# Kernel tuning notes

Measured on AMD Instinct MI355X. Metric: run time of the kernel, lower is better.

Reference implementation:

```python
import jax, jax.numpy as jnp
import numpy as np

B, S, DIN, DQ, DK, NGL = 4, 8192, 512, 512, 512, 64


def setup_inputs() -> dict:
    key = jax.random.key(0)
    ks = jax.random.split(key, 10)
    q = jax.random.normal(ks[0], (B, S, DIN), dtype=jnp.float32)
    k = jax.random.normal(ks[1], (B, S, DIN), dtype=jnp.float32)
    v = jax.random.normal(ks[2], (B, S, DIN), dtype=jnp.float32)
    sc_in = 1.0 / np.sqrt(DIN)
    Wq = jax.random.normal(ks[3], (DQ, DIN), dtype=jnp.float32) * sc_in
    bq = jax.random.normal(ks[4], (DQ,), dtype=jnp.float32) * 0.01
    Wk = jax.random.normal(ks[5], (DK, DIN), dtype=jnp.float32) * sc_in
    bk = jax.random.normal(ks[6], (DK,), dtype=jnp.float32) * 0.01
    Wv = jax.random.normal(ks[7], (DK, DIN), dtype=jnp.float32) * sc_in
    bv = jax.random.normal(ks[8], (DK,), dtype=jnp.float32) * 0.01
    # deterministic stand-in for random.sample(range(DK), NGL): unique indices
    rng = np.random.default_rng(0)
    global_tokens = jnp.asarray(rng.choice(DK, size=NGL, replace=False), dtype=jnp.int32)
    return {"q": q, "k": k, "v": v, "Wq": Wq, "bq": bq, "Wk": Wk, "bk": bk,
            "Wv": Wv, "bv": bv, "global_tokens": global_tokens}


def _make_mask(global_tokens):
    # mask[a, b] = -inf iff a < b and neither a nor b is a global token
    idx = jnp.arange(DK)
    glb = jnp.zeros((DK,), dtype=bool).at[global_tokens].set(True)
    cond = (idx[:, None] < idx[None, :]) & (~glb[:, None]) & (~glb[None, :])
    return jnp.where(cond, -jnp.inf, 0.0).astype(jnp.float32)  # [DQ, DK]


def reference(q, k, v, Wq, bq, Wk, bk, Wv, bv, global_tokens):
    Q = q @ Wq.T + bq            # [B, S, DQ]
    K = k @ Wk.T + bk            # [B, S, DK]
    V = v @ Wv.T + bv            # [B, S, DK]
    # num = Q^T K contracting over the sequence axis -> [B, DQ, DK]
    num = jnp.einsum('bsq,bsk->bqk', Q, K)
    mask = _make_mask(global_tokens)
    denom = jnp.asarray(DK, jnp.float32) ** 0.5
    attn = jax.nn.softmax((num + mask) / denom, axis=-1)  # [B, DQ, DK]
    # attn @ V^T -> [B, DQ, S]
    out = jnp.einsum('bqk,bsk->bqs', attn, V)
    return out
```

## Files before the change

kernel.cpp:

```cpp
#include <hip/hip_runtime.h>
#include <stdint.h>

typedef short short8 __attribute__((ext_vector_type(8)));
typedef short short4v __attribute__((ext_vector_type(4)));
typedef float f32x4 __attribute__((ext_vector_type(4)));
typedef unsigned short ushort_t;

__device__ __forceinline__ void barrier_lds(){
  asm volatile("s_waitcnt lgkmcnt(0)\n\ts_barrier" ::: "memory");
}

__device__ __forceinline__ unsigned short bf16_rne(float x){
  unsigned int u = __float_as_uint(x);
  return (unsigned short)((u + 0x7FFFu + ((u >> 16) & 1u)) >> 16);
}
__device__ __forceinline__ unsigned cvt_pk(float a, float b){
  unsigned r;
  asm("v_cvt_pk_bf16_f32 %0, %1, %2" : "=v"(r) : "v"(a), "v"(b));
  return r;
}
__device__ __forceinline__ void split4(float a0, float a1, float a2, float a3,
                                       unsigned &h0, unsigned &h1,
                                       unsigned &l0, unsigned &l1){
  h0 = cvt_pk(a0, a1); h1 = cvt_pk(a2, a3);
  float f0 = __uint_as_float(h0 << 16), f1 = __uint_as_float(h0 & 0xFFFF0000u);
  float f2 = __uint_as_float(h1 << 16), f3 = __uint_as_float(h1 & 0xFFFF0000u);
  l0 = cvt_pk(a0 - f0, a1 - f1); l1 = cvt_pk(a2 - f2, a3 - f3);
}
__device__ __forceinline__ uint4 hi8(float4 x, float4 y){
  uint4 h; h.x = cvt_pk(x.x, x.y); h.y = cvt_pk(x.z, x.w);
  h.z = cvt_pk(y.x, y.y); h.w = cvt_pk(y.z, y.w); return h;
}
__device__ __forceinline__ void split8(float4 x, float4 y, uint4 &h, uint4 &l){
  split4(x.x, x.y, x.z, x.w, h.x, h.y, l.x, l.y);
  split4(y.x, y.y, y.z, y.w, h.z, h.w, l.z, l.w);
}
__device__ __forceinline__ short8 comb(short4v a, short4v b){
  short8 r; r[0]=a[0]; r[1]=a[1]; r[2]=a[2]; r[3]=a[3];
  r[4]=b[0]; r[5]=b[1]; r[6]=b[2]; r[7]=b[3]; return r;
}

template<int TS, int ABF, int BBF, int NT, int EPI, int OB>
__global__ __launch_bounds__(256, 2) void gemm_bt(
    const void* __restrict__ Av, const void* __restrict__ Bv,
    void* __restrict__ Cv, const float* __restrict__ cvec,
    int tn, int K, int lda, int ldb, int ldc,
    long sA, long sB, long sC, long scv)
{
  const int bz = blockIdx.y;
  const int mt = blockIdx.x / tn, nt = blockIdx.x % tn;
  const int m0 = mt * TS, n0 = nt * TS;

  constexpr int MI   = TS / 64;
  constexpr int ROWE = TS * 32;
  constexpr int PL   = (NT == 3) ? 2 * ROWE : ROWE;
  constexpr int TBYT = 4 * PL;
  constexpr int SB   = (2 * TBYT > 16384) ? 2 * TBYT : 16384;
  constexpr int EL   = (TS == 128) ? 16 : 8;
  __shared__ __align__(16) char SMEM[SB];
  short* Ah  = (short*)SMEM;
  short* Bh2 = (short*)(SMEM + TBYT);
  float* EP  = (float*)SMEM;

  const int t = threadIdx.x;
  const int lane = t & 63, wid = t >> 6;
  const int rowS = (TS == 128) ? (t >> 1) : (t >> 2);
  const int kh   = (TS == 128) ? (t & 1)  : (t & 3);
  const int wr = wid >> 1, wc = wid & 1;
  const int fr = lane & 15, fg = lane >> 4;

  f32x4 acc[2*MI][2*MI];
  const f32x4 Z = {0.f, 0.f, 0.f, 0.f};
  #pragma unroll
  for (int i = 0; i < 2*MI; i++)
    #pragma unroll
    for (int j = 0; j < 2*MI; j++) acc[i][j] = Z;

  const int wbase = rowS * 32;
  const int sw = (rowS >> 1) & 3;
  const int i0 = wbase + ((((TS == 128) ? (kh << 1) : kh) ^ sw) << 3);
  const int i1 = (TS == 128) ? (wbase + ((((kh << 1) + 1) ^ sw) << 3)) : 0;

  const float*    Afp = (const float*)Av    + sA * bz + (long)(m0 + rowS) * lda + kh * EL;
  const ushort_t* Abp = (const ushort_t*)Av + sA * bz + (long)(m0 + rowS) * lda + kh * EL;
  const float*    Bfp = (const float*)Bv    + sB * bz + (long)(n0 + rowS) * ldb + kh * EL;
  const ushort_t* Bbp = (const ushort_t*)Bv + sB * bz + (long)(n0 + rowS) * ldb + kh * EL;

  struct Pf { float4 v[4]; };
  struct Ps { short8 v[2]; };
  Pf Af[2], Bf[2]; Ps As8[2], Bs8[2];

  auto loadA = [&](int s, int kk){
    if (ABF == 0){
      const float4* p = (const float4*)(Afp + kk);
      Af[s].v[0] = p[0]; Af[s].v[1] = p[1];
      if (TS == 128){ Af[s].v[2] = p[2]; Af[s].v[3] = p[3]; }
    } else {
      const short8* p = (const short8*)(Abp + kk);
      As8[s].v[0] = p[0]; if (TS == 128) As8[s].v[1] = p[1];
    }
  };
  auto loadB = [&](int s, int kk){
    if (BBF == 0){
      const float4* p = (const float4*)(Bfp + kk);
      Bf[s].v[0] = p[0]; Bf[s].v[1] = p[1];
      if (TS == 128){ Bf[s].v[2] = p[2]; Bf[s].v[3] = p[3]; }
    } else {
      const short8* p = (const short8*)(Bbp + kk);
      Bs8[s].v[0] = p[0]; if (TS == 128) Bs8[s].v[1] = p[1];
    }
  };

  auto stage = [&](int s){
    const int off = s * PL;
    if (ABF == 0){
      if (NT == 3){
        uint4 h0, l0; split8(Af[s].v[0], Af[s].v[1], h0, l0);
        *(uint4*)&Ah[off + i0] = h0; *(uint4*)&Ah[off + i0 + ROWE] = l0;
        if (TS == 128){
          uint4 h1, l1; split8(Af[s].v[2], Af[s].v[3], h1, l1);
          *(uint4*)&Ah[off + i1] = h1; *(uint4*)&Ah[off + i1 + ROWE] = l1;
        }
      } else {
        *(uint4*)&Ah[off + i0] = hi8(Af[s].v[0], Af[s].v[1]);
        if (TS == 128) *(uint4*)&Ah[off + i1] = hi8(Af[s].v[2], Af[s].v[3]);
      }
    } else {
      *(short8*)&Ah[off + i0] = As8[s].v[0];
      if (TS == 128) *(short8*)&Ah[off + i1] = As8[s].v[1];
    }
    if (BBF == 0){
      if (NT == 3){
        uint4 h0, l0; split8(Bf[s].v[0], Bf[s].v[1], h0, l0);
        *(uint4*)&Bh2[off + i0] = h0; *(uint4*)&Bh2[off + i0 + ROWE] = l0;
        if (TS == 128){
          uint4 h1, l1; split8(Bf[s].v[2], Bf[s].v[3], h1, l1);
          *(uint4*)&Bh2[off + i1] = h1; *(uint4*)&Bh2[off + i1 + ROWE] = l1;
        }
      } else {
        *(uint4*)&Bh2[off + i0] = hi8(Bf[s].v[0], Bf[s].v[1]);
        if (TS == 128) *(uint4*)&Bh2[off + i1] = hi8(Bf[s].v[2], Bf[s].v[3]);
      }
    } else {
      *(short8*)&Bh2[off + i0] = Bs8[s].v[0];
      if (TS == 128) *(short8*)&Bh2[off + i1] = Bs8[s].v[1];
    }
  };

  loadA(0, 0); loadB(0, 0); loadA(1, 32); loadB(1, 32);

  for (int k0 = 0; k0 < K; k0 += 64){
    barrier_lds();
    stage(0);
    { int kn = (k0 + 64 < K) ? (k0 + 64) : k0;       loadA(0, kn); loadB(0, kn); }
    stage(1);
    { int kn = (k0 + 64 < K) ? (k0 + 96) : (k0 + 32); loadA(1, kn); loadB(1, kn); }
    barrier_lds();

    #pragma unroll
    for (int s = 0; s < 2; s++){
      const int off = s * PL;
      short8 fa[2*MI], fb[2*MI], fal[2*MI], fbl[2*MI];
      #pragma unroll
      for (int mi = 0; mi < 2*MI; mi++){
        int r = wr * (32*MI) + mi * 16 + fr;
        int idx = off + r * 32 + ((fg ^ ((r >> 1) & 3)) << 3);
        fa[mi] = *(const short8*)&Ah[idx];
        if (NT == 3) fal[mi] = *(const short8*)&Ah[idx + ROWE];
      }
      #pragma unroll
      for (int ni = 0; ni < 2*MI; ni++){
        int r = wc * (32*MI) + ni * 16 + fr;
        int idx = off + r * 32 + ((fg ^ ((r >> 1) & 3)) << 3);
        fb[ni] = *(const short8*)&Bh2[idx];
        if (NT == 3) fbl[ni] = *(const short8*)&Bh2[idx + ROWE];
      }
      #pragma unroll
      for (int mi = 0; mi < 2*MI; mi++)
        #pragma unroll
        for (int ni = 0; ni < 2*MI; ni++){
          acc[mi][ni] = __builtin_amdgcn_mfma_f32_16x16x32_bf16(fa[mi], fb[ni], acc[mi][ni], 0, 0, 0);
          if (NT == 3){
            acc[mi][ni] = __builtin_amdgcn_mfma_f32_16x16x32_bf16(fal[mi], fb[ni],  acc[mi][ni], 0, 0, 0);
            acc[mi][ni] = __builtin_amdgcn_mfma_f32_16x16x32_bf16(fa[mi],  fbl[ni], acc[mi][ni], 0, 0, 0);
          }
        }
    }
  }

  float*    Cf = (float*)Cv    + sC * bz;
  ushort_t* Cb = (ushort_t*)Cv + sC * bz;
  if (TS == 128){
    #pragma unroll
    for (int p = 0; p < 4; p++){
      __syncthreads();
      if (wr == (p >> 1)){
        #pragma unroll
        for (int m2 = 0; m2 < 2; m2++){
          int mi = 2 * (p & 1) + m2;
          #pragma unroll
          for (int ni = 0; ni < 4; ni++)
            #pragma unroll
            for (int j = 0; j < 4; j++){
              int lr = m2 * 16 + fg * 4 + j;
              float o = acc[mi][ni][j];
              if (EPI == 1) o += cvec[scv * bz + m0 + p * 32 + lr];
              EP[lr * 128 + wc * 64 + ni * 16 + fr] = o;
            }
        }
      }
      __syncthreads();
      const int row = t >> 3, seg = t & 7;
      const float* src = EP + row * 128 + seg * 16;
      if (OB == 1){
        ushort_t* dst = Cb + (long)(m0 + p * 32 + row) * ldc + n0 + seg * 16;
        uint4 o0, o1;
        o0.x = cvt_pk(src[0], src[1]);  o0.y = cvt_pk(src[2], src[3]);
        o0.z = cvt_pk(src[4], src[5]);  o0.w = cvt_pk(src[6], src[7]);
        o1.x = cvt_pk(src[8], src[9]);  o1.y = cvt_pk(src[10], src[11]);
        o1.z = cvt_pk(src[12], src[13]); o1.w = cvt_pk(src[14], src[15]);
        *(uint4*)dst = o0; *(uint4*)(dst + 8) = o1;
      } else {
        float* dst = Cf + (long)(m0 + p * 32 + row) * ldc + n0 + seg * 16;
        #pragma unroll
        for (int c = 0; c < 4; c++)
          *(float4*)(dst + c * 4) = *(const float4*)(src + c * 4);
      }
    }
  } else {
    __syncthreads();
    #pragma unroll
    for (int mi = 0; mi < 2; mi++)
      #pragma unroll
      for (int ni = 0; ni < 2; ni++)
        #pragma unroll
        for (int j = 0; j < 4; j++){
          int lr = wr * 32 + mi * 16 + fg * 4 + j;
          float o = acc[mi][ni][j];
          if (EPI == 1) o += cvec[scv * bz + m0 + lr];
          EP[lr * 64 + wc * 32 + ni * 16 + fr] = o;
        }
    __syncthreads();
    const int row = t >> 2, seg = t & 3;
    const float* src = EP + row * 64 + seg * 16;
    if (OB == 1){
      ushort_t* dst = Cb + (long)(m0 + row) * ldc + n0 + seg * 16;
      uint4 o0, o1;
      o0.x = cvt_pk(src[0], src[1]);  o0.y = cvt_pk(src[2], src[3]);
      o0.z = cvt_pk(src[4], src[5]);  o0.w = cvt_pk(src[6], src[7]);
      o1.x = cvt_pk(src[8], src[9]);  o1.y = cvt_pk(src[10], src[11]);
      o1.z = cvt_pk(src[12], src[13]); o1.w = cvt_pk(src[14], src[15]);
      *(uint4*)dst = o0; *(uint4*)(dst + 8) = o1;
    } else {
      float* dst = Cf + (long)(m0 + row) * ldc + n0 + seg * 16;
      #pragma unroll
      for (int c = 0; c < 4; c++)
        *(float4*)(dst + c * 4) = *(const float4*)(src + c * 4);
    }
  }
}

template<int NSP>
__global__ __launch_bounds__(256, 2) void gemm1_tn(
    const float* __restrict__ q, const float* __restrict__ k,
    float* __restrict__ mtp, float* __restrict__ sqp, float* __restrict__ skp)
{
  constexpr int CH = 8192 / NSP;
  constexpr int STEPS = CH / 64;
  const int b = blockIdx.z, sp = blockIdx.y;
  const int mt = blockIdx.x >> 2, nt = blockIdx.x & 3;
  const float* qb = q + (long)b * 8192 * 512;
  const float* kb = k + (long)b * 8192 * 512;

  __shared__ __align__(16) char SMEM[65536];
  unsigned char* As = (unsigned char*)SMEM;
  unsigned char* Bs = (unsigned char*)(SMEM + 32768);

  const int t = threadIdx.x;
  const int lam = t & 31, sg = t >> 5;
  const int lane = t & 63, wid = t >> 6;
  const int wr = wid >> 1, wc = wid & 1;
  const int fr = lane & 15, fg = lane >> 4;

  f32x4 acc[4][4];
  const f32x4 Z = {0.f, 0.f, 0.f, 0.f};
  #pragma unroll
  for (int i = 0; i < 4; i++)
    #pragma unroll
    for (int j = 0; j < 4; j++) acc[i][j] = Z;

  float sumk4[4] = {0.f, 0.f, 0.f, 0.f};
  float sumq4[4] = {0.f, 0.f, 0.f, 0.f};

  int wA[4];
  #pragma unroll
  for (int j = 0; j < 4; j++){
    int c = lam * 4 + j;
    int swc = ((c >> 2) ^ ((c & 3) << 1)) & 7;
    wA[j] = c * 128 + ((sg ^ swc) << 4);
  }

  const float* kbase = kb + (long)(sp * CH + sg * 4) * 512 + mt * 128 + lam * 4;
  const float* qbase = qb + (long)(sp * CH + sg * 4) * 512 + nt * 128 + lam * 4;

  struct Pf { float4 v[4]; };
  Pf Kf[2], Qf[2];

  auto ldK = [&](int s, int st){
    const float* p = kbase + (long)(st * 64 + s * 32) * 512;
    Kf[s].v[0] = *(const float4*)(p);
    Kf[s].v[1] = *(const float4*)(p + 512);
    Kf[s].v[2] = *(const float4*)(p + 1024);
    Kf[s].v[3] = *(const float4*)(p + 1536);
  };
  auto ldQ = [&](int s, int st){
    const float* p = qbase + (long)(st * 64 + s * 32) * 512;
    Qf[s].v[0] = *(const float4*)(p);
    Qf[s].v[1] = *(const float4*)(p + 512);
    Qf[s].v[2] = *(const float4*)(p + 1024);
    Qf[s].v[3] = *(const float4*)(p + 1536);
  };

  auto cvK = [&](int s){
    #pragma unroll
    for (int j = 0; j < 4; j++){
      float a0 = ((const float*)&Kf[s].v[0])[j], a1 = ((const float*)&Kf[s].v[1])[j];
      float a2 = ((const float*)&Kf[s].v[2])[j], a3 = ((const float*)&Kf[s].v[3])[j];
      sumk4[j] += (a0 + a1) + (a2 + a3);
      unsigned h0, h1, l0, l1;
      split4(a0, a1, a2, a3, h0, h1, l0, l1);
      uint4 w; w.x = h0; w.y = h1; w.z = l0; w.w = l1;
      *(uint4*)(As + s * 16384 + wA[j]) = w;
    }
  };
  auto cvQ = [&](int s){
    #pragma unroll
    for (int j = 0; j < 4; j++){
      float a0 = ((const float*)&Qf[s].v[0])[j], a1 = ((const float*)&Qf[s].v[1])[j];
      float a2 = ((const float*)&Qf[s].v[2])[j], a3 = ((const float*)&Qf[s].v[3])[j];
      sumq4[j] += (a0 + a1) + (a2 + a3);
      uint2 w2; w2.x = cvt_pk(a0, a1); w2.y = cvt_pk(a2, a3);
      *(uint2*)(Bs + s * 16384 + wA[j]) = w2;
    }
  };

  ldK(0, 0); ldQ(0, 0); ldK(1, 0); ldQ(1, 0);

  for (int st = 0; st < STEPS; ++st){
    barrier_lds();
    cvK(0); cvQ(0);
    { int ns = (st < STEPS - 1) ? (st + 1) : st; ldK(0, ns); ldQ(0, ns); }
    cvK(1); cvQ(1);
    { int ns = (st < STEPS - 1) ? (st + 1) : st; ldK(1, ns); ldQ(1, ns); }
    barrier_lds();

    #pragma unroll
    for (int s = 0; s < 2; s++){
      const unsigned char* Ab = As + s * 16384;
      const unsigned char* Bb = Bs + s * 16384;
      short8 fa[4], fal[4], fb[4];
      #pragma unroll
      for (int mi = 0; mi < 4; mi++){
        int r = wr * 64 + mi * 16 + fr;
        int swc = ((r >> 2) ^ ((r & 3) << 1)) & 7;
        const unsigned char* bp = Ab + r * 128;
        int u0 = (((fg << 1) + 0) ^ swc) << 4;
        int u1 = (((fg << 1) + 1) ^ swc) << 4;
        fa[mi]  = comb(*(const short4v*)(bp + u0),     *(const short4v*)(bp + u1));
        fal[mi] = comb(*(const short4v*)(bp + u0 + 8), *(const short4v*)(bp + u1 + 8));
      }
      #pragma unroll
      for (int ni = 0; ni < 4; ni++){
        int r = wc * 64 + ni * 16 + fr;
        int swc = ((r >> 2) ^ ((r & 3) << 1)) & 7;
        const unsigned char* bp = Bb + r * 128;
        int u0 = (((fg << 1) + 0) ^ swc) << 4;
        int u1 = (((fg << 1) + 1) ^ swc) << 4;
        fb[ni]  = comb(*(const short4v*)(bp + u0), *(const short4v*)(bp + u1));
      }
      #pragma unroll
      for (int mi = 0; mi < 4; mi++)
        #pragma unroll
        for (int ni = 0; ni < 4; ni++){
          acc[mi][ni] = __builtin_amdgcn_mfma_f32_16x16x32_bf16(fa[mi],  fb[ni], acc[mi][ni], 0, 0, 0);
          acc[mi][ni] = __builtin_amdgcn_mfma_f32_16x16x32_bf16(fal[mi], fb[ni], acc[mi][ni], 0, 0, 0);
        }
    }
  }

  float* Cp = mtp + ((long)sp * 4 + b) * (512 * 512);
  #pragma unroll
  for (int mi = 0; mi < 4; mi++)
    #pragma unroll
    for (int ni = 0; ni < 4; ni++){
      int gr0 = mt * 128 + wr * 64 + mi * 16 + fg * 4;
      int gc  = nt * 128 + wc * 64 + ni * 16 + fr;
      #pragma unroll
      for (int j = 0; j < 4; j++)
        Cp[(long)(gr0 + j) * 512 + gc] = acc[mi][ni][j];
    }

  __syncthreads();
  float* red = (float*)SMEM;
  if (mt == 0){
    #pragma unroll
    for (int j = 0; j < 4; j++) red[sg * 128 + lam * 4 + j] = sumq4[j];
    __syncthreads();
    if (t < 128){
      float s2 = 0.f;
      #pragma unroll
      for (int gg = 0; gg < 8; gg++) s2 += red[gg * 128 + t];
      sqp[((long)b * NSP + sp) * 512 + nt * 128 + t] = s2;
    }
    __syncthreads();
  }
  if (nt == 0){
    #pragma unroll
    for (int j = 0; j < 4; j++) red[sg * 128 + lam * 4 + j] = sumk4[j];
    __syncthreads();
    if (t < 128){
      float s2 = 0.f;
      #pragma unroll
      for (int gg = 0; gg < 8; gg++) s2 += red[gg * 128 + t];
      skp[((long)b * NSP + sp) * 512 + mt * 128 + t] = s2;
    }
  }
}

template<int NS>
__global__ __launch_bounds__(256) void reduceM(float* __restrict__ p){
  const int bid = blockIdx.x;
  const int b = bid >> 8;
  const long i = (long)(bid & 255) * 1024 + threadIdx.x * 4;
  float4 s = {0.f, 0.f, 0.f, 0.f};
  #pragma unroll
  for (int j = 0; j < NS; j++){
    float4 v = *(const float4*)(p + ((long)j * 4 + b) * 262144 + i);
    s.x += v.x; s.y += v.y; s.z += v.z; s.w += v.w;
  }
  *(float4*)(p + (long)b * 262144 + i) = s;
}

__global__ __launch_bounds__(256) void transpose512(const float* __restrict__ in, float* __restrict__ outp){
  __shared__ float tile[32][33];
  const int bx = blockIdx.x & 15, by = blockIdx.x >> 4;
  const int tx = threadIdx.x & 31, ty = threadIdx.x >> 5;
  #pragma unroll
  for (int r = 0; r < 4; r++)
    tile[ty + 8*r][tx] = in[(long)(by*32 + ty + 8*r) * 512 + bx*32 + tx];
  __syncthreads();
  #pragma unroll
  for (int r = 0; r < 4; r++)
    outp[(long)(bx*32 + ty + 8*r) * 512 + by*32 + tx] = tile[tx][ty + 8*r];
}

__global__ __launch_bounds__(256) void smallprep(
    const float* __restrict__ sqp, const float* __restrict__ skp,
    const float* __restrict__ Wq, const float* __restrict__ Wk,
    float* __restrict__ wqsq, float* __restrict__ wksk, int nsp)
{
  const int bid = blockIdx.x;
  const int tau = bid >> 4;
  const int b = (bid >> 2) & 3, ab = bid & 3;
  const float* P = tau ? skp : sqp;
  const float* W = tau ? Wk : Wq;
  float* O = tau ? wksk : wqsq;
  __shared__ float sv[512];
  const int t = threadIdx.x;
  for (int i = t; i < 512; i += 256){
    float s = 0.f;
    for (int g = 0; g < nsp; g++) s += P[((long)b * nsp + g) * 512 + i];
    sv[i] = s;
  }
  __syncthreads();
  const int a = ab * 128 + (t >> 1), half = t & 1;
  const float* Wr = W + (long)a * 512 + half * 256;
  const float* sp2 = sv + half * 256;
  float d = 0.f;
  #pragma unroll 8
  for (int j = 0; j < 256; j++) d += Wr[j] * sp2[j];
  d += __shfl_xor(d, 1);
  if (!half) O[(long)b * 512 + a] = d;
}

__global__ __launch_bounds__(256) void softmax_k(
    const float* __restrict__ num, float* __restrict__ attn, float* __restrict__ cv,
    const float* __restrict__ wqsq, const float* __restrict__ wksk,
    const float* __restrict__ bq, const float* __restrict__ bk,
    const float* __restrict__ bv, const int* __restrict__ gt)
{
  const int a = blockIdx.x, b = blockIdx.y;
  const int t = threadIdx.x;
  const int lane = t & 63, wid = t >> 6;
  __shared__ unsigned char gf[512];
  __shared__ float red[4];
  gf[t] = 0; gf[t + 256] = 0;
  __syncthreads();
  if (t < 64) gf[gt[t]] = 1;
  __syncthreads();

  const float* row = num + ((long)b * 512 + a) * 512;
  const float bqa = bq[a], wqa = wqsq[b * 512 + a];
  const int ga = gf[a];
  const int c0 = t, c1 = t + 256;
  float l0 = (row[c0] + wqa * bk[c0] + bqa * wksk[b*512 + c0] + 8192.0f * bqa * bk[c0]) * 0.04419417382415922f;
  float l1 = (row[c1] + wqa * bk[c1] + bqa * wksk[b*512 + c1] + 8192.0f * bqa * bk[c1]) * 0.04419417382415922f;
  if (a < c0 && !ga && !gf[c0]) l0 = -1e30f;
  if (a < c1 && !ga && !gf[c1]) l1 = -1e30f;

  float m = fmaxf(l0, l1);
  #pragma unroll
  for (int o = 32; o; o >>= 1) m = fmaxf(m, __shfl_xor(m, o));
  if (lane == 0) red[wid] = m;
  __syncthreads();
  m = fmaxf(fmaxf(red[0], red[1]), fmaxf(red[2], red[3]));
  __syncthreads();

  float e0 = __expf(l0 - m), e1 = __expf(l1 - m);
  float s = e0 + e1;
  #pragma unroll
  for (int o = 32; o; o >>= 1) s += __shfl_xor(s, o);
  if (lane == 0) red[wid] = s;
  __syncthreads();
  s = red[0] + red[1] + red[2] + red[3];
  __syncthreads();
  const float inv = 1.0f / s;
  const float a0 = e0 * inv, a1 = e1 * inv;
  float* arow = attn + ((long)b * 512 + a) * 512;
  arow[c0] = a0; arow[c1] = a1;

  float cp = a0 * bv[c0] + a1 * bv[c1];
  #pragma unroll
  for (int o = 32; o; o >>= 1) cp += __shfl_xor(cp, o);
  if (lane == 0) red[wid] = cp;
  __syncthreads();
  if (t == 0) cv[(long)b * 512 + a] = red[0] + red[1] + red[2] + red[3];
}

extern "C" void kernel_launch(void* const* d_in, const int* in_sizes, int n_in,
                              void* d_out, int out_size, void* d_ws, size_t ws_size,
                              hipStream_t stream) {
  const float* q  = (const float*)d_in[0];
  const float* k  = (const float*)d_in[1];
  const float* v  = (const float*)d_in[2];
  const float* Wq = (const float*)d_in[3];
  const float* bq = (const float*)d_in[4];
  const float* Wk = (const float*)d_in[5];
  const float* bk = (const float*)d_in[6];
  const float* Wv = (const float*)d_in[7];
  const float* bv = (const float*)d_in[8];
  const int*   gt = (const int*)d_in[9];
  float* out = (float*)d_out;

  const int NSP = 8;

  float* w = (float*)d_ws;
  float* MT   = w;
  float* T1   = w + 1048576;
  float* NUM  = w + 2097152;
  float* ATT  = w + 3145728;
  float* A2H  = w + 4194304;
  float* WVT  = A2H + 524288;
  float* SM   = w + 8L * 1048576;
  float* SQP  = SM;
  float* SKP  = SQP + 32768;
  float* WQS  = SKP + 32768;
  float* WKS  = WQS + 2048;
  float* CV   = WKS + 2048;
  ushort_t* a2h = (ushort_t*)A2H;

  gemm1_tn<8><<<dim3(16, 8, 4), 256, 0, stream>>>(q, k, w, SQP, SKP);
  reduceM<8><<<1024, 256, 0, stream>>>(w);
  transpose512<<<256, 256, 0, stream>>>(Wv, WVT);
  smallprep<<<32, 256, 0, stream>>>(SQP, SKP, Wq, Wk, WQS, WKS, NSP);
  gemm_bt<64,0,0,3,0,0><<<dim3(64, 4), 256, 0, stream>>>(Wq, MT, T1, nullptr,
      8, 512, 512, 512, 512, 0L, 262144L, 262144L, 0L);
  gemm_bt<64,0,0,3,0,0><<<dim3(64, 4), 256, 0, stream>>>(T1, Wk, NUM, nullptr,
      8, 512, 512, 512, 512, 262144L, 0L, 262144L, 0L);
  softmax_k<<<dim3(512, 4), 256, 0, stream>>>(NUM, ATT, CV, WQS, WKS, bq, bk, bv, gt);
  gemm_bt<64,0,0,1,0,1><<<dim3(64, 4), 256, 0, stream>>>(ATT, WVT, a2h, nullptr,
      8, 512, 512, 512, 512, 262144L, 0L, 262144L, 0L);
  gemm_bt<128,1,0,1,1,0><<<dim3(256, 4), 256, 0, stream>>>(a2h, v, out, CV,
      64, 512, 512, 512, 8192, 262144L, 4194304L, 4194304L, 512L);
}
```

Baseline: 193.9 us.

## Fuse softmax into attn-times-Wv GEMM and merge prep kernels into one launch

Three small prep kernels (partial-sum reduction, Wv transpose, bias-correction dot products) are merged into one launch that dispatches on block index. The softmax kernel and the following attn×WvT GEMM are fused: each block recomputes softmax for its 64 rows, writes unnormalised bf16 probabilities into LDS and runs MFMA against the transposed Wv, normalising at the epilogue. This removes two launches and the fp32 attention matrix round trip through global memory. The cost is that softmax work is redone by all eight column tiles, plus a large LDS footprint that limits occupancy. There is also an apparent ordering risk: the merged prep kernel produces the transposed Wv and the sum vectors in the same launch that reads the reduced buffers, so it relies on block independence.

Measured after the change: 205.8 us. +6.1%, slower.

```diff
diff --git a/kernel.cpp b/kernel.cpp
--- a/kernel.cpp
+++ b/kernel.cpp
@@ -428,113 +428,225 @@
 }
 
 template<int NS>
-__global__ __launch_bounds__(256) void reduceM(float* __restrict__ p){
-  const int bid = blockIdx.x;
-  const int b = bid >> 8;
-  const long i = (long)(bid & 255) * 1024 + threadIdx.x * 4;
-  float4 s = {0.f, 0.f, 0.f, 0.f};
-  #pragma unroll
-  for (int j = 0; j < NS; j++){
-    float4 v = *(const float4*)(p + ((long)j * 4 + b) * 262144 + i);
-    s.x += v.x; s.y += v.y; s.z += v.z; s.w += v.w;
-  }
-  *(float4*)(p + (long)b * 262144 + i) = s;
-}
-
-__global__ __launch_bounds__(256) void transpose512(const float* __restrict__ in, float* __restrict__ outp){
-  __shared__ float tile[32][33];
-  const int bx = blockIdx.x & 15, by = blockIdx.x >> 4;
-  const int tx = threadIdx.x & 31, ty = threadIdx.x >> 5;
-  #pragma unroll
-  for (int r = 0; r < 4; r++)
-    tile[ty + 8*r][tx] = in[(long)(by*32 + ty + 8*r) * 512 + bx*32 + tx];
-  __syncthreads();
-  #pragma unroll
-  for (int r = 0; r < 4; r++)
-    outp[(long)(bx*32 + ty + 8*r) * 512 + by*32 + tx] = tile[tx][ty + 8*r];
-}
-
-__global__ __launch_bounds__(256) void smallprep(
+__global__ __launch_bounds__(256) void midprep(
+    float* __restrict__ p,
+    const float* __restrict__ Wv, float* __restrict__ wvT,
     const float* __restrict__ sqp, const float* __restrict__ skp,
     const float* __restrict__ Wq, const float* __restrict__ Wk,
-    float* __restrict__ wqsq, float* __restrict__ wksk, int nsp)
+    float* __restrict__ wqsq, float* __restrict__ wksk)
 {
+  __shared__ float shm[33 * 32];
   const int bid = blockIdx.x;
-  const int tau = bid >> 4;
-  const int b = (bid >> 2) & 3, ab = bid & 3;
-  const float* P = tau ? skp : sqp;
-  const float* W = tau ? Wk : Wq;
-  float* O = tau ? wksk : wqsq;
-  __shared__ float sv[512];
   const int t = threadIdx.x;
-  for (int i = t; i < 512; i += 256){
-    float s = 0.f;
-    for (int g = 0; g < nsp; g++) s += P[((long)b * nsp + g) * 512 + i];
-    sv[i] = s;
-  }
-  __syncthreads();
-  const int a = ab * 128 + (t >> 1), half = t & 1;
-  const float* Wr = W + (long)a * 512 + half * 256;
-  const float* sp2 = sv + half * 256;
-  float d = 0.f;
-  #pragma unroll 8
-  for (int j = 0; j < 256; j++) d += Wr[j] * sp2[j];
-  d += __shfl_xor(d, 1);
-  if (!half) O[(long)b * 512 + a] = d;
-}
-
-__global__ __launch_bounds__(256) void softmax_k(
-    const float* __restrict__ num, float* __restrict__ attn, float* __restrict__ cv,
+  if (bid < 1024){
+    const int b = bid >> 8;
+    const long i = (long)(bid & 255) * 1024 + t * 4;
+    float4 s = {0.f, 0.f, 0.f, 0.f};
+    #pragma unroll
+    for (int j = 0; j < NS; j++){
+      float4 v = *(const float4*)(p + ((long)j * 4 + b) * 262144 + i);
+      s.x += v.x; s.y += v.y; s.z += v.z; s.w += v.w;
+    }
+    *(float4*)(p + (long)b * 262144 + i) = s;
+  } else if (bid < 1280){
+    const int bb = bid - 1024;
+    const int bx = bb & 15, by = bb >> 4;
+    const int tx = t & 31, ty = t >> 5;
+    float (*tile)[33] = (float(*)[33])shm;
+    #pragma unroll
+    for (int r = 0; r < 4; r++)
+      tile[ty + 8*r][tx] = Wv[(long)(by*32 + ty + 8*r) * 512 + bx*32 + tx];
+    __syncthreads();
+    #pragma unroll
+    for (int r = 0; r < 4; r++)
+      wvT[(long)(bx*32 + ty + 8*r) * 512 + by*32 + tx] = tile[tx][ty + 8*r];
+  } else {
+    const int bb = bid - 1280;
+    const int tau = bb >> 4;
+    const int b = (bb >> 2) & 3, ab = bb & 3;
+    const float* P = tau ? skp : sqp;
+    const float* W = tau ? Wk : Wq;
+    float* O = tau ? wksk : wqsq;
+    float* sv = shm;
+    for (int i = t; i < 512; i += 256){
+      float s = 0.f;
+      #pragma unroll
+      for (int g = 0; g < NS; g++) s += P[((long)b * NS + g) * 512 + i];
+      sv[i] = s;
+    }
+    __syncthreads();
+    const int a = ab * 128 + (t >> 1), half = t & 1;
+    const float* Wr = W + (long)a * 512 + half * 256;
+    const float* sp2 = sv + half * 256;
+    float d = 0.f;
+    #pragma unroll 8
+    for (int j = 0; j < 256; j++) d += Wr[j] * sp2[j];
+    d += __shfl_xor(d, 1);
+    if (!half) O[(long)b * 512 + a] = d;
+  }
+}
+
+__global__ __launch_bounds__(256, 2) void a2_fused(
+    const float* __restrict__ num, const float* __restrict__ wvT,
+    ushort_t* __restrict__ a2h, float* __restrict__ cv,
     const float* __restrict__ wqsq, const float* __restrict__ wksk,
     const float* __restrict__ bq, const float* __restrict__ bk,
     const float* __restrict__ bv, const int* __restrict__ gt)
 {
-  const int a = blockIdx.x, b = blockIdx.y;
+  const int b = blockIdx.y;
+  const int mt = blockIdx.x >> 3, nt = blockIdx.x & 7;
+  const int a0 = mt * 64, n0 = nt * 64;
+
+  __shared__ __align__(16) short Pl[16 * 2048];
+  __shared__ __align__(16) short Bh2[2 * 2048];
+  __shared__ unsigned char gf[512];
+  __shared__ unsigned gfb[16];
+  __shared__ float sarr[64], cvarr[64];
+
   const int t = threadIdx.x;
   const int lane = t & 63, wid = t >> 6;
-  __shared__ unsigned char gf[512];
-  __shared__ float red[4];
+  const int wr = wid >> 1, wc = wid & 1;
+  const int fr = lane & 15, fg = lane >> 4;
+
   gf[t] = 0; gf[t + 256] = 0;
   __syncthreads();
   if (t < 64) gf[gt[t]] = 1;
   __syncthreads();
-
-  const float* row = num + ((long)b * 512 + a) * 512;
+  if (t < 16){
+    unsigned m2 = 0;
+    #pragma unroll
+    for (int j = 0; j < 32; j++) m2 |= ((unsigned)gf[t * 32 + j]) << j;
+    gfb[t] = m2;
+  }
+  __syncthreads();
+
+  const int row = t >> 2;
+  const int a = a0 + row;
+  const int cs = (t & 3) * 128;
+  const float* nrow = num + ((long)b * 512 + a) * 512;
+  const float* wkrow = wksk + b * 512;
   const float bqa = bq[a], wqa = wqsq[b * 512 + a];
-  const int ga = gf[a];
-  const int c0 = t, c1 = t + 256;
-  float l0 = (row[c0] + wqa * bk[c0] + bqa * wksk[b*512 + c0] + 8192.0f * bqa * bk[c0]) * 0.04419417382415922f;
-  float l1 = (row[c1] + wqa * bk[c1] + bqa * wksk[b*512 + c1] + 8192.0f * bqa * bk[c1]) * 0.04419417382415922f;
-  if (a < c0 && !ga && !gf[c0]) l0 = -1e30f;
-  if (a < c1 && !ga && !gf[c1]) l1 = -1e30f;
-
-  float m = fmaxf(l0, l1);
+  const bool maskable = (gf[a] == 0);
+  unsigned gm[4];
   #pragma unroll
-  for (int o = 32; o; o >>= 1) m = fmaxf(m, __shfl_xor(m, o));
-  if (lane == 0) red[wid] = m;
+  for (int j = 0; j < 4; j++) gm[j] = gfb[(cs >> 5) + j];
+  const float SCL = 0.04419417382415922f;
+
+  float m = -1e30f;
+  for (int c8 = cs; c8 < cs + 128; c8 += 8){
+    float4 nv0 = *(const float4*)(nrow + c8),  nv1 = *(const float4*)(nrow + c8 + 4);
+    float4 bk0 = *(const float4*)(bk + c8),    bk1 = *(const float4*)(bk + c8 + 4);
+    float4 wk0 = *(const float4*)(wkrow + c8), wk1 = *(const float4*)(wkrow + c8 + 4);
+    #pragma unroll
+    for (int j = 0; j < 8; j++){
+      int c = c8 + j;
+      float nvv = (j < 4) ? ((const float*)&nv0)[j] : ((const float*)&nv1)[j-4];
+      float bkv = (j < 4) ? ((const float*)&bk0)[j] : ((const float*)&bk1)[j-4];
+      float wkv = (j < 4) ? ((const float*)&wk0)[j] : ((const float*)&wk1)[j-4];
+      float l = (nvv + wqa * bkv + bqa * wkv + 8192.0f * bqa * bkv) * SCL;
+      bool msk = (a < c) && maskable && !((gm[(c - cs) >> 5] >> (c & 31)) & 1u);
+      if (msk) l = -1e30f;
+      m = fmaxf(m, l);
+    }
+  }
+  m = fmaxf(m, __shfl_xor(m, 1));
+  m = fmaxf(m, __shfl_xor(m, 2));
+
+  float ssum = 0.f, cpart = 0.f;
+  for (int c8 = cs; c8 < cs + 128; c8 += 8){
+    float4 nv0 = *(const float4*)(nrow + c8),  nv1 = *(const float4*)(nrow + c8 + 4);
+    float4 bk0 = *(const float4*)(bk + c8),    bk1 = *(const float4*)(bk + c8 + 4);
+    float4 wk0 = *(const float4*)(wkrow + c8), wk1 = *(const float4*)(wkrow + c8 + 4);
+    float4 bv0 = *(const float4*)(bv + c8),    bv1 = *(const float4*)(bv + c8 + 4);
+    float e[8];
+    #pragma unroll
+    for (int j = 0; j < 8; j++){
+      int c = c8 + j;
+      float nvv = (j < 4) ? ((const float*)&nv0)[j] : ((const float*)&nv1)[j-4];
+      float bkv = (j < 4) ? ((const float*)&bk0)[j] : ((const float*)&bk1)[j-4];
+      float wkv = (j < 4) ? ((const float*)&wk0)[j] : ((const float*)&wk1)[j-4];
+      float bvv = (j < 4) ? ((const float*)&bv0)[j] : ((const float*)&bv1)[j-4];
+      float l = (nvv + wqa * bkv + bqa * wkv + 8192.0f * bqa * bkv) * SCL;
+      bool msk = (a < c) && maskable && !((gm[(c - cs) >> 5] >> (c & 31)) & 1u);
+      if (msk) l = -1e30f;
+      float ev = __expf(l - m);
+      e[j] = ev; ssum += ev; cpart += ev * bvv;
+    }
+    const int sub = c8 >> 5;
+    const int slot = ((c8 & 31) >> 3) ^ ((row >> 1) & 3);
+    uint4 w4;
+    w4.x = cvt_pk(e[0], e[1]); w4.y = cvt_pk(e[2], e[3]);
+    w4.z = cvt_pk(e[4], e[5]); w4.w = cvt_pk(e[6], e[7]);
+    *(uint4*)&Pl[sub * 2048 + row * 32 + slot * 8] = w4;
+  }
+  ssum  += __shfl_xor(ssum, 1);  ssum  += __shfl_xor(ssum, 2);
+  cpart += __shfl_xor(cpart, 1); cpart += __shfl_xor(cpart, 2);
+  if ((t & 3) == 0){ sarr[row] = ssum; cvarr[row] = cpart; }
   __syncthreads();
-  m = fmaxf(fmaxf(red[0], red[1]), fmaxf(red[2], red[3]));
-  __syncthreads();
-
-  float e0 = __expf(l0 - m), e1 = __expf(l1 - m);
-  float s = e0 + e1;
+  if (nt == 0 && t < 64) cv[(long)b * 512 + a0 + t] = cvarr[t] / sarr[t];
+
+  f32x4 acc[2][2];
+  const f32x4 Z = {0.f, 0.f, 0.f, 0.f};
+  acc[0][0] = Z; acc[0][1] = Z; acc[1][0] = Z; acc[1][1] = Z;
+
+  const int rowS = t >> 2, kh = t & 3;
+  const int ib = rowS * 32 + ((kh ^ ((rowS >> 1) & 3)) << 3);
+  const float* Bfp = wvT + (long)(n0 + rowS) * 512 + kh * 8;
+
+  struct Pf2 { float4 v[2]; };
+  Pf2 Bf[2];
+  auto ldB = [&](int s, int kk){
+    const float4* p = (const float4*)(Bfp + kk);
+    Bf[s].v[0] = p[0]; Bf[s].v[1] = p[1];
+  };
+  auto stB = [&](int s){
+    *(uint4*)&Bh2[s * 2048 + ib] = hi8(Bf[s].v[0], Bf[s].v[1]);
+  };
+
+  ldB(0, 0); ldB(1, 32);
+
+  for (int k0 = 0; k0 < 512; k0 += 64){
+    barrier_lds();
+    stB(0);
+    { int kn = (k0 + 64 < 512) ? (k0 + 64) : k0;        ldB(0, kn); }
+    stB(1);
+    { int kn = (k0 + 64 < 512) ? (k0 + 96) : (k0 + 32); ldB(1, kn); }
+    barrier_lds();
+
+    #pragma unroll
+    for (int s = 0; s < 2; s++){
+      const int sub = (k0 >> 5) + s;
+      short8 fa[2], fb[2];
+      #pragma unroll
+      for (int mi = 0; mi < 2; mi++){
+        int r = wr * 32 + mi * 16 + fr;
+        fa[mi] = *(const short8*)&Pl[sub * 2048 + r * 32 + ((fg ^ ((r >> 1) & 3)) << 3)];
+      }
+      #pragma unroll
+      for (int ni = 0; ni < 2; ni++){
+        int r = wc * 32 + ni * 16 + fr;
+        fb[ni] = *(const short8*)&Bh2[s * 2048 + r * 32 + ((fg ^ ((r >> 1) & 3)) << 3)];
+      }
+      #pragma unroll
+      for (int mi = 0; mi < 2; mi++)
+        #pragma unroll
+        for (int ni = 0; ni < 2; ni++)
+          acc[mi][ni] = __builtin_amdgcn_mfma_f32_16x16x32_bf16(fa[mi], fb[ni], acc[mi][ni], 0, 0, 0);
+    }
+  }
+
   #pragma unroll
-  for (int o = 32; o; o >>= 1) s += __shfl_xor(s, o);
-  if (lane == 0) red[wid] = s;
-  __syncthreads();
-  s = red[0] + red[1] + red[2] + red[3];
-  __syncthreads();
-  const float inv = 1.0f / s;
-  const float a0 = e0 * inv, a1 = e1 * inv;
-  float* arow = attn + ((long)b * 512 + a) * 512;
-  arow[c0] = a0; arow[c1] = a1;
-
-  float cp = a0 * bv[c0] + a1 * bv[c1];
-  #pragma unroll
-  for (int o = 32; o; o >>= 1) cp += __shfl_xor(cp, o);
-  if (lane == 0) red[wid] = cp;
-  __syncthreads();
-  if (t == 0) cv[(long)b * 512 + a] = red[0] + red[1] + red[2] + red[3];
+  for (int mi = 0; mi < 2; mi++)
+    #pragma unroll
+    for (int ni = 0; ni < 2; ni++){
+      int lr0 = wr * 32 + mi * 16 + fg * 4;
+      int gc  = n0 + wc * 32 + ni * 16 + fr;
+      #pragma unroll
+      for (int j = 0; j < 4; j++){
+        float o = acc[mi][ni][j] / sarr[lr0 + j];
+        a2h[(long)b * 262144 + (long)(a0 + lr0 + j) * 512 + gc] = bf16_rne(o);
+      }
+    }
 }
 
 extern "C" void kernel_launch(void* const* d_in, const int* in_sizes, int n_in,
@@ -552,13 +664,10 @@
   const int*   gt = (const int*)d_in[9];
   float* out = (float*)d_out;
 
-  const int NSP = 8;
-
   float* w = (float*)d_ws;
   float* MT   = w;
   float* T1   = w + 1048576;
   float* NUM  = w + 2097152;
-  float* ATT  = w + 3145728;
   float* A2H  = w + 4194304;
   float* WVT  = A2H + 524288;
   float* SM   = w + 8L * 1048576;
@@ -570,16 +679,13 @@
   ushort_t* a2h = (ushort_t*)A2H;
 
   gemm1_tn<8><<<dim3(16, 8, 4), 256, 0, stream>>>(q, k, w, SQP, SKP);
-  reduceM<8><<<1024, 256, 0, stream>>>(w);
-  transpose512<<<256, 256, 0, stream>>>(Wv, WVT);
-  smallprep<<<32, 256, 0, stream>>>(SQP, SKP, Wq, Wk, WQS, WKS, NSP);
+  midprep<8><<<1312, 256, 0, stream>>>(w, Wv, WVT, SQP, SKP, Wq, Wk, WQS, WKS);
   gemm_bt<64,0,0,3,0,0><<<dim3(64, 4), 256, 0, stream>>>(Wq, MT, T1, nullptr,
       8, 512, 512, 512, 512, 0L, 262144L, 262144L, 0L);
   gemm_bt<64,0,0,3,0,0><<<dim3(64, 4), 256, 0, stream>>>(T1, Wk, NUM, nullptr,
       8, 512, 512, 512, 512, 262144L, 0L, 262144L, 0L);
-  softmax_k<<<dim3(512, 4), 256, 0, stream>>>(NUM, ATT, CV, WQS, WKS, bq, bk, bv, gt);
-  gemm_bt<64,0,0,1,0,1><<<dim3(64, 4), 256, 0, stream>>>(ATT, WVT, a2h, nullptr,
-      8, 512, 512, 512, 512, 262144L, 0L, 262144L, 0L);
+  a2_fused<<<dim3(64, 4), 256, 0, stream>>>(NUM, WVT, a2h, CV,
+      WQS, WKS, bq, bk, bv, gt);
   gemm_bt<128,1,0,1,1,0><<<dim3(256, 4), 256, 0, stream>>>(a2h, v, out, CV,
       64, 512, 512, 512, 8192, 262144L, 4194304L, 4194304L, 512L);
 }
```
